# Performance work log

Measured on AMD Instinct MI355X. Metric: run time of the kernel, lower is better.

The kernel has to match this reference:

```python
import jax, jax.numpy as jnp
import numpy as np
from jax import lax

B, T, I, H = 64, 2048, 64, 256


def setup_inputs() -> dict:
    key = jax.random.key(0)
    ks = jax.random.split(key, 7)
    s = 1.0 / np.sqrt(H)  # PyTorch LSTM/Linear init scale
    x = jax.random.normal(ks[0], (B, T, I), dtype=jnp.float32)
    W_ih = jax.random.uniform(ks[1], (4 * H, I), minval=-s, maxval=s, dtype=jnp.float32)
    W_hh = jax.random.uniform(ks[2], (4 * H, H), minval=-s, maxval=s, dtype=jnp.float32)
    b_ih = jax.random.uniform(ks[3], (4 * H,), minval=-s, maxval=s, dtype=jnp.float32)
    b_hh = jax.random.uniform(ks[4], (4 * H,), minval=-s, maxval=s, dtype=jnp.float32)
    W_o = jax.random.uniform(ks[5], (1, H), minval=-s, maxval=s, dtype=jnp.float32)
    b_o = jax.random.uniform(ks[6], (1,), minval=-s, maxval=s, dtype=jnp.float32)
    return {"x": x, "W_ih": W_ih, "W_hh": W_hh, "b_ih": b_ih, "b_hh": b_hh, "W_o": W_o, "b_o": b_o}


def _lstm(x, W_ih, W_hh, b_ih, b_hh):
    # x: [B, T, I]. PyTorch gate order: i, f, g, o.
    Bn, Tn, _ = x.shape
    Hn = W_hh.shape[1]
    # Precompute input contribution for all timesteps (one big GEMM).
    gx = jnp.einsum('bti,gi->btg', x, W_ih) + b_ih + b_hh  # [B, T, 4H]

    def step(carry, gxt):
        h, c = carry
        gates = gxt + h @ W_hh.T  # [B, 4H]
        i, f, g, o = jnp.split(gates, 4, axis=-1)
        c = jax.nn.sigmoid(f) * c + jax.nn.sigmoid(i) * jnp.tanh(g)
        h = jax.nn.sigmoid(o) * jnp.tanh(c)
        return (h, c), h

    h0 = jnp.zeros((Bn, Hn), x.dtype)
    (_, _), hs = lax.scan(step, (h0, h0), jnp.swapaxes(gx, 0, 1))  # hs: [T, B, H]
    return jnp.swapaxes(hs, 0, 1)  # [B, T, H]


def reference(x, W_ih, W_hh, b_ih, b_hh, W_o, b_o):
    hs = _lstm(x, W_ih, W_hh, b_ih, b_hh)          # [B, T, H]
    return hs @ W_o.T + b_o                         # [B, T, 1]
```

## Files before the change

### kernel.cpp

```cpp
#include <hip/hip_runtime.h>
#include <hip/hip_fp16.h>

#define B_  64
#define T_  2048
#define I_  64
#define H_  256
#define G4_ 1024

typedef _Float16 h2v __attribute__((ext_vector_type(2)));

__device__ __forceinline__ float fdot2(uint32_t a, uint32_t b, float c) {
#if __has_builtin(__builtin_amdgcn_fdot2)
    return __builtin_amdgcn_fdot2(__builtin_bit_cast(h2v, a), __builtin_bit_cast(h2v, b), c, false);
#else
    h2v ha = __builtin_bit_cast(h2v, a), hb = __builtin_bit_cast(h2v, b);
    return c + (float)ha.x * (float)hb.x + (float)ha.y * (float)hb.y;
#endif
}

__device__ __forceinline__ ushort f2h(float v) {
    return __builtin_bit_cast(ushort, (_Float16)v);
}
__device__ __forceinline__ float h2f(ushort v) {
    return (float)__builtin_bit_cast(_Float16, v);
}

__global__ void repack_kernel(const float* __restrict__ Whh, ushort* __restrict__ wpk) {
    int o  = blockIdx.x * 256 + threadIdx.x;
    int j  = o & 7;
    int h  = (o >> 3) & 255;
    int kc = (o >> 11) & 31;
    int g  = o >> 16;
    float v = Whh[(g * 256 + h) * 256 + kc * 8 + j];
    wpk[o] = f2h(v);
}

__global__ __launch_bounds__(256) void gx_kernel(
    const float* __restrict__ x, const float* __restrict__ Wih,
    const float* __restrict__ bih, const float* __restrict__ bhh,
    ushort* __restrict__ gx, int t0, int TCc) {

    __shared__ float xs[32][64];
    const int bt0 = blockIdx.x * 32;
    const int row = blockIdx.y * 256 + threadIdx.x;

    for (int i = threadIdx.x; i < 512; i += 256) {
        int r  = i >> 4, c4 = i & 15;
        int bt = bt0 + r;
        int b  = bt / TCc;
        int tl = bt - b * TCc;
        *(float4*)(&xs[r][c4 * 4]) =
            *(const float4*)(&x[(((size_t)b * T_) + t0 + tl) * I_ + c4 * 4]);
    }
    __syncthreads();

    float w[64];
#pragma unroll
    for (int k = 0; k < 64; ++k) w[k] = Wih[row * I_ + k];
    const float bias = bih[row] + bhh[row];

    for (int i = 0; i < 32; ++i) {
        float acc = bias;
#pragma unroll
        for (int k4 = 0; k4 < 16; ++k4) {
            float4 xq = *(const float4*)(&xs[i][k4 * 4]);
            acc = fmaf(w[k4 * 4 + 0], xq.x, acc);
            acc = fmaf(w[k4 * 4 + 1], xq.y, acc);
            acc = fmaf(w[k4 * 4 + 2], xq.z, acc);
            acc = fmaf(w[k4 * 4 + 3], xq.w, acc);
        }
        gx[(size_t)(bt0 + i) * G4_ + row] = f2h(acc);
    }
}

__global__ __attribute__((amdgpu_flat_work_group_size(512, 512), amdgpu_waves_per_eu(2, 2)))
void lstm_kernel(
    const ushort* __restrict__ wpk, const ushort* __restrict__ gx,
    ushort* __restrict__ hbuf,
    float* __restrict__ state,
    int TCc, int first) {

    __shared__ __align__(16) ushort wg4[256 * 256];
    __shared__ __align__(16) ushort hs[256];
    __shared__ __align__(16) float pex[256][4];

    const int tid   = threadIdx.x;
    const int hd    = tid & 255;
    const int q     = tid >> 8;
    const int kbase = q << 4;
    const int tmask = hd & 31;
    const int b     = blockIdx.x;
    const bool q0   = (q == 0);

    uint32_t wi[64], wf[64], wg[64];
#pragma unroll
    for (int k = 0; k < 16; ++k) {
        uint4 v = *(const uint4*)(wpk + (size_t)(0 * 32 + kbase + k) * 2048 + hd * 8);
        wi[k * 4 + 0] = v.x; wi[k * 4 + 1] = v.y; wi[k * 4 + 2] = v.z; wi[k * 4 + 3] = v.w;
    }
#pragma unroll
    for (int k = 0; k < 16; ++k) {
        uint4 v = *(const uint4*)(wpk + (size_t)(1 * 32 + kbase + k) * 2048 + hd * 8);
        wf[k * 4 + 0] = v.x; wf[k * 4 + 1] = v.y; wf[k * 4 + 2] = v.z; wf[k * 4 + 3] = v.w;
    }
#pragma unroll
    for (int k = 0; k < 16; ++k) {
        uint4 v = *(const uint4*)(wpk + (size_t)(2 * 32 + kbase + k) * 2048 + hd * 8);
        wg[k * 4 + 0] = v.x; wg[k * 4 + 1] = v.y; wg[k * 4 + 2] = v.z; wg[k * 4 + 3] = v.w;
    }
#pragma unroll
    for (int k = 0; k < 16; ++k) {
        uint4 v = *(const uint4*)(wpk + (size_t)(3 * 32 + kbase + k) * 2048 + hd * 8);
        int u = (kbase + k) ^ tmask;
        *(uint4*)(wg4 + hd * 256 + u * 8) = v;
    }

    float c = 0.f, h = 0.f;
    if (q0) {
        if (!first) {
            c = state[b * H_ + hd];
            h = state[B_ * H_ + b * H_ + hd];
        }
        hs[hd] = f2h(h);
    }
    __syncthreads();

    const ushort* gxb = gx + (size_t)b * TCc * G4_;
    ushort* hb = hbuf + (size_t)b * TCc * H_;

    ushort c_i = 0, c_f = 0, c_g = 0, c_o = 0;
    if (q0) {
        c_i = gxb[hd]; c_f = gxb[256 + hd]; c_g = gxb[512 + hd]; c_o = gxb[768 + hd];
    }

    for (int tl = 0; tl < TCc; ++tl) {
        ushort n_i = 0, n_f = 0, n_g = 0, n_o = 0;
        if (q0) {
            const int tn = (tl + 1 < TCc) ? tl + 1 : tl;
            const size_t nb = (size_t)tn * G4_;
            n_i = gxb[nb + hd];       n_f = gxb[nb + 256 + hd];
            n_g = gxb[nb + 512 + hd]; n_o = gxb[nb + 768 + hd];
        }

        float ai, af, ag, ao;
        if (q0) { ai = h2f(c_i); af = h2f(c_f); ag = h2f(c_g); ao = h2f(c_o); }
        else    { ai = 0.f; af = 0.f; ag = 0.f; ao = 0.f; }

#pragma unroll
        for (int k = 0; k < 16; ++k) {
            const int kc = kbase + k;
            uint4 hq = *(const uint4*)(hs + kc * 8);
            int u = kc ^ tmask;
            uint4 wo = *(const uint4*)(wg4 + hd * 256 + u * 8);
            ai = fdot2(wi[k * 4 + 0], hq.x, ai);
            ai = fdot2(wi[k * 4 + 1], hq.y, ai);
            ai = fdot2(wi[k * 4 + 2], hq.z, ai);
            ai = fdot2(wi[k * 4 + 3], hq.w, ai);
            af = fdot2(wf[k * 4 + 0], hq.x, af);
            af = fdot2(wf[k * 4 + 1], hq.y, af);
            af = fdot2(wf[k * 4 + 2], hq.z, af);
            af = fdot2(wf[k * 4 + 3], hq.w, af);
            ag = fdot2(wg[k * 4 + 0], hq.x, ag);
            ag = fdot2(wg[k * 4 + 1], hq.y, ag);
            ag = fdot2(wg[k * 4 + 2], hq.z, ag);
            ag = fdot2(wg[k * 4 + 3], hq.w, ag);
            ao = fdot2(wo.x, hq.x, ao);
            ao = fdot2(wo.y, hq.y, ao);
            ao = fdot2(wo.z, hq.z, ao);
            ao = fdot2(wo.w, hq.w, ao);
        }

        if (!q0) {
            pex[hd][0] = ai; pex[hd][1] = af; pex[hd][2] = ag; pex[hd][3] = ao;
        }
        __syncthreads();

        if (q0) {
            float4 px = *(const float4*)(&pex[hd][0]);
            ai += px.x; af += px.y; ag += px.z; ao += px.w;

            float si = __builtin_amdgcn_rcpf(1.f + __expf(-ai));
            float sf = __builtin_amdgcn_rcpf(1.f + __expf(-af));
            float so = __builtin_amdgcn_rcpf(1.f + __expf(-ao));
            float eg = __expf(2.f * ag);
            float tg = (eg - 1.f) * __builtin_amdgcn_rcpf(eg + 1.f);
            c = sf * c + si * tg;
            float ec = __expf(2.f * c);
            float tc = (ec - 1.f) * __builtin_amdgcn_rcpf(ec + 1.f);
            h = so * tc;

            ushort hh = f2h(h);
            hs[hd] = hh;
            hb[(size_t)tl * H_ + hd] = hh;
        }
        __syncthreads();

        c_i = n_i; c_f = n_f; c_g = n_g; c_o = n_o;
    }

    if (q0) {
        state[b * H_ + hd]            = c;
        state[B_ * H_ + b * H_ + hd]  = h;
    }
}

__global__ __launch_bounds__(256) void proj_kernel(
    const ushort* __restrict__ hbuf, const float* __restrict__ Wo,
    const float* __restrict__ bo, float* __restrict__ out, int t0, int TCc) {

    const int lane = threadIdx.x & 63;
    const int wid  = blockIdx.x * 4 + (threadIdx.x >> 6);
    const int nw   = gridDim.x * 4;
    const int rows = B_ * TCc;

    float4 w = *(const float4*)(Wo + lane * 4);
    const float bov = bo[0];

    for (int r = wid; r < rows; r += nw) {
        const ushort* hp = hbuf + (size_t)r * H_ + lane * 4;
        ushort4 u = *(const ushort4*)hp;
        float p = h2f(u.x) * w.x + h2f(u.y) * w.y + h2f(u.z) * w.z + h2f(u.w) * w.w;
#pragma unroll
        for (int m = 1; m < 64; m <<= 1) p += __shfl_xor(p, m, 64);
        if (lane == 0) {
            int b  = r / TCc;
            int tl = r - b * TCc;
            out[(size_t)b * T_ + t0 + tl] = p + bov;
        }
    }
}

extern "C" void kernel_launch(void* const* d_in, const int* in_sizes, int n_in,
                              void* d_out, int out_size, void* d_ws, size_t ws_size,
                              hipStream_t stream) {
    const float* x   = (const float*)d_in[0];
    const float* Wih = (const float*)d_in[1];
    const float* Whh = (const float*)d_in[2];
    const float* bih = (const float*)d_in[3];
    const float* bhh = (const float*)d_in[4];
    const float* Wo  = (const float*)d_in[5];
    const float* bo  = (const float*)d_in[6];
    float* out = (float*)d_out;

    char* ws = (char*)d_ws;
    ushort* wpk   = (ushort*)ws;
    float*  state = (float*)(ws + 512 * 1024);
    char*   dyn   = ws + 640 * 1024;

    size_t avail = (ws_size > 640 * 1024) ? ws_size - 640 * 1024 : 0;
    long long tcmax = (long long)(avail / ((size_t)B_ * (G4_ + H_) * 2));
    int TC = (tcmax > T_) ? T_ : (int)tcmax;
    TC &= ~63;
    if (TC < 64) TC = 64;

    repack_kernel<<<1024, 256, 0, stream>>>(Whh, wpk);

    for (int t0 = 0; t0 < T_; t0 += TC) {
        int TCc = (T_ - t0 < TC) ? (T_ - t0) : TC;
        ushort* gxb  = (ushort*)dyn;
        ushort* hbuf = (ushort*)(dyn + (size_t)B_ * TCc * G4_ * 2);
        dim3 g1((B_ * TCc) / 32, 4);
        gx_kernel<<<g1, 256, 0, stream>>>(x, Wih, bih, bhh, gxb, t0, TCc);
        lstm_kernel<<<B_, 512, 0, stream>>>(wpk, gxb, hbuf, state, TCc, t0 == 0 ? 1 : 0);
        proj_kernel<<<256, 256, 0, stream>>>(hbuf, Wo, bo, out, t0, TCc);
    }
    (void)in_sizes; (void)n_in; (void)out_size;
}
```

Before: 3.448 ms.

## Move part of o-gate weights to registers and cap time chunk size

The o-gate weights are split so that 4 of each thread's 16 k-chunks sit in registers and the other 12 sit in LDS. The LDS layout changes from an XOR-swizzled per-row layout to a [k][q][hd] layout. This cuts per-step LDS reads for the o-gate and shrinks shared memory, at the cost of 16 more VGPRs per thread. The time chunk is also capped at 512 steps, so the gx/lstm/proj kernels run over several chunks instead of one, which may keep the gx buffer in cache but adds launches.

```diff
diff --git a/kernel.cpp b/kernel.cpp
--- a/kernel.cpp
+++ b/kernel.cpp
@@ -80,7 +80,7 @@
     float* __restrict__ state,
     int TCc, int first) {
 
-    __shared__ __align__(16) ushort wg4[256 * 256];
+    __shared__ __align__(16) ushort wg4[12 * 2 * 256 * 8];
     __shared__ __align__(16) ushort hs[256];
     __shared__ __align__(16) float pex[256][4];
 
@@ -88,7 +88,6 @@
     const int hd    = tid & 255;
     const int q     = tid >> 8;
     const int kbase = q << 4;
-    const int tmask = hd & 31;
     const int b     = blockIdx.x;
     const bool q0   = (q == 0);
 
@@ -109,10 +108,15 @@
         wg[k * 4 + 0] = v.x; wg[k * 4 + 1] = v.y; wg[k * 4 + 2] = v.z; wg[k * 4 + 3] = v.w;
     }
 #pragma unroll
-    for (int k = 0; k < 16; ++k) {
+    for (int k = 0; k < 12; ++k) {
         uint4 v = *(const uint4*)(wpk + (size_t)(3 * 32 + kbase + k) * 2048 + hd * 8);
-        int u = (kbase + k) ^ tmask;
-        *(uint4*)(wg4 + hd * 256 + u * 8) = v;
+        *(uint4*)(wg4 + ((k * 2 + q) * 256 + hd) * 8) = v;
+    }
+    uint32_t wo_r[16];
+#pragma unroll
+    for (int k = 0; k < 4; ++k) {
+        uint4 v = *(const uint4*)(wpk + (size_t)(3 * 32 + kbase + 12 + k) * 2048 + hd * 8);
+        wo_r[k * 4 + 0] = v.x; wo_r[k * 4 + 1] = v.y; wo_r[k * 4 + 2] = v.z; wo_r[k * 4 + 3] = v.w;
     }
 
     float c = 0.f, h = 0.f;
@@ -147,11 +151,10 @@
         else    { ai = 0.f; af = 0.f; ag = 0.f; ao = 0.f; }
 
 #pragma unroll
-        for (int k = 0; k < 16; ++k) {
+        for (int k = 0; k < 12; ++k) {
             const int kc = kbase + k;
             uint4 hq = *(const uint4*)(hs + kc * 8);
-            int u = kc ^ tmask;
-            uint4 wo = *(const uint4*)(wg4 + hd * 256 + u * 8);
+            uint4 wo = *(const uint4*)(wg4 + ((k * 2 + q) * 256 + hd) * 8);
             ai = fdot2(wi[k * 4 + 0], hq.x, ai);
             ai = fdot2(wi[k * 4 + 1], hq.y, ai);
             ai = fdot2(wi[k * 4 + 2], hq.z, ai);
@@ -169,6 +172,28 @@
             ao = fdot2(wo.z, hq.z, ao);
             ao = fdot2(wo.w, hq.w, ao);
         }
+#pragma unroll
+        for (int k = 12; k < 16; ++k) {
+            const int kc = kbase + k;
+            const int r  = (k - 12) * 4;
+            uint4 hq = *(const uint4*)(hs + kc * 8);
+            ai = fdot2(wi[k * 4 + 0], hq.x, ai);
+            ai = fdot2(wi[k * 4 + 1], hq.y, ai);
+            ai = fdot2(wi[k * 4 + 2], hq.z, ai);
+            ai = fdot2(wi[k * 4 + 3], hq.w, ai);
+            af = fdot2(wf[k * 4 + 0], hq.x, af);
+            af = fdot2(wf[k * 4 + 1], hq.y, af);
+            af = fdot2(wf[k * 4 + 2], hq.z, af);
+            af = fdot2(wf[k * 4 + 3], hq.w, af);
+            ag = fdot2(wg[k * 4 + 0], hq.x, ag);
+            ag = fdot2(wg[k * 4 + 1], hq.y, ag);
+            ag = fdot2(wg[k * 4 + 2], hq.z, ag);
+            ag = fdot2(wg[k * 4 + 3], hq.w, ag);
+            ao = fdot2(wo_r[r + 0], hq.x, ao);
+            ao = fdot2(wo_r[r + 1], hq.y, ao);
+            ao = fdot2(wo_r[r + 2], hq.z, ao);
+            ao = fdot2(wo_r[r + 3], hq.w, ao);
+        }
 
         if (!q0) {
             pex[hd][0] = ai; pex[hd][1] = af; pex[hd][2] = ag; pex[hd][3] = ao;
@@ -249,7 +274,7 @@
 
     size_t avail = (ws_size > 640 * 1024) ? ws_size - 640 * 1024 : 0;
     long long tcmax = (long long)(avail / ((size_t)B_ * (G4_ + H_) * 2));
-    int TC = (tcmax > T_) ? T_ : (int)tcmax;
+    int TC = (tcmax > 512) ? 512 : (int)tcmax;
     TC &= ~63;
     if (TC < 64) TC = 64;
 
```

Result: slower. 3.878 ms (+12.5%).

## Split LSTM K-reduction across 4 lanes with shuffles and double-buffered hidden state

Applied to the files above, without the earlier changes.

Each recurrent block now uses 1024 threads: four adjacent lanes share one hidden unit and each covers a quarter of K. Their partial dot products are combined with wave shuffles instead of a shared-memory exchange, which removes one barrier per timestep. The hidden state is double-buffered in padded shared memory, and the gate preactivations are stored interleaved so each thread reads all four with one 8-byte load. The time chunk is capped at 512, giving more kernel launches, and every lane now computes the redundant activation math.

```diff
diff --git a/kernel.cpp b/kernel.cpp
--- a/kernel.cpp
+++ b/kernel.cpp
@@ -38,11 +38,12 @@
 __global__ __launch_bounds__(256) void gx_kernel(
     const float* __restrict__ x, const float* __restrict__ Wih,
     const float* __restrict__ bih, const float* __restrict__ bhh,
-    ushort* __restrict__ gx, int t0, int TCc) {
+    ushort* __restrict__ gx2, int t0, int TCc) {
 
     __shared__ float xs[32][64];
     const int bt0 = blockIdx.x * 32;
-    const int row = blockIdx.y * 256 + threadIdx.x;
+    const int gq  = blockIdx.y;
+    const int row = gq * 256 + threadIdx.x;
 
     for (int i = threadIdx.x; i < 512; i += 256) {
         int r  = i >> 4, c4 = i & 15;
@@ -69,138 +70,126 @@
             acc = fmaf(w[k4 * 4 + 2], xq.z, acc);
             acc = fmaf(w[k4 * 4 + 3], xq.w, acc);
         }
-        gx[(size_t)(bt0 + i) * G4_ + row] = f2h(acc);
-    }
-}
-
-__global__ __attribute__((amdgpu_flat_work_group_size(512, 512), amdgpu_waves_per_eu(2, 2)))
+        gx2[((size_t)(bt0 + i) * 256 + threadIdx.x) * 4 + gq] = f2h(acc);
+    }
+}
+
+__global__ __attribute__((amdgpu_flat_work_group_size(1024, 1024)))
 void lstm_kernel(
-    const ushort* __restrict__ wpk, const ushort* __restrict__ gx,
+    const ushort* __restrict__ wpk, const ushort* __restrict__ gx2,
     ushort* __restrict__ hbuf,
     float* __restrict__ state,
     int TCc, int first) {
 
     __shared__ __align__(16) ushort wg4[256 * 256];
-    __shared__ __align__(16) ushort hs[256];
-    __shared__ __align__(16) float pex[256][4];
-
-    const int tid   = threadIdx.x;
-    const int hd    = tid & 255;
-    const int q     = tid >> 8;
-    const int kbase = q << 4;
-    const int tmask = hd & 31;
-    const int b     = blockIdx.x;
-    const bool q0   = (q == 0);
-
-    uint32_t wi[64], wf[64], wg[64];
-#pragma unroll
-    for (int k = 0; k < 16; ++k) {
-        uint4 v = *(const uint4*)(wpk + (size_t)(0 * 32 + kbase + k) * 2048 + hd * 8);
+    __shared__ __align__(16) ushort hs[2][288];
+
+    const int tid = threadIdx.x;
+    const int q   = tid & 3;
+    const int hd  = tid >> 2;
+    const int hm  = hd & 31;
+    const int b   = blockIdx.x;
+
+    uint32_t wi[32], wf[32], wg[32];
+#pragma unroll
+    for (int k = 0; k < 8; ++k) {
+        uint4 v = *(const uint4*)(wpk + (size_t)(0 * 32 + q * 8 + k) * 2048 + hd * 8);
         wi[k * 4 + 0] = v.x; wi[k * 4 + 1] = v.y; wi[k * 4 + 2] = v.z; wi[k * 4 + 3] = v.w;
     }
 #pragma unroll
-    for (int k = 0; k < 16; ++k) {
-        uint4 v = *(const uint4*)(wpk + (size_t)(1 * 32 + kbase + k) * 2048 + hd * 8);
+    for (int k = 0; k < 8; ++k) {
+        uint4 v = *(const uint4*)(wpk + (size_t)(1 * 32 + q * 8 + k) * 2048 + hd * 8);
         wf[k * 4 + 0] = v.x; wf[k * 4 + 1] = v.y; wf[k * 4 + 2] = v.z; wf[k * 4 + 3] = v.w;
     }
 #pragma unroll
-    for (int k = 0; k < 16; ++k) {
-        uint4 v = *(const uint4*)(wpk + (size_t)(2 * 32 + kbase + k) * 2048 + hd * 8);
+    for (int k = 0; k < 8; ++k) {
+        uint4 v = *(const uint4*)(wpk + (size_t)(2 * 32 + q * 8 + k) * 2048 + hd * 8);
         wg[k * 4 + 0] = v.x; wg[k * 4 + 1] = v.y; wg[k * 4 + 2] = v.z; wg[k * 4 + 3] = v.w;
     }
 #pragma unroll
-    for (int k = 0; k < 16; ++k) {
-        uint4 v = *(const uint4*)(wpk + (size_t)(3 * 32 + kbase + k) * 2048 + hd * 8);
-        int u = (kbase + k) ^ tmask;
+    for (int k = 0; k < 8; ++k) {
+        uint4 v = *(const uint4*)(wpk + (size_t)(3 * 32 + q * 8 + k) * 2048 + hd * 8);
+        int u = (q * 8 + k) ^ hm;
         *(uint4*)(wg4 + hd * 256 + u * 8) = v;
     }
 
     float c = 0.f, h = 0.f;
-    if (q0) {
-        if (!first) {
-            c = state[b * H_ + hd];
-            h = state[B_ * H_ + b * H_ + hd];
-        }
-        hs[hd] = f2h(h);
+    if (!first) {
+        c = state[b * H_ + hd];
+        h = state[B_ * H_ + b * H_ + hd];
+    }
+    if (q == 0) {
+        int sw = ((hd >> 3) + (hd >> 6)) * 8 + (hd & 7);
+        hs[0][sw] = f2h(h);
     }
     __syncthreads();
 
-    const ushort* gxb = gx + (size_t)b * TCc * G4_;
+    const ushort* gxb = gx2 + (size_t)b * TCc * G4_;
     ushort* hb = hbuf + (size_t)b * TCc * H_;
 
-    ushort c_i = 0, c_f = 0, c_g = 0, c_o = 0;
-    if (q0) {
-        c_i = gxb[hd]; c_f = gxb[256 + hd]; c_g = gxb[512 + hd]; c_o = gxb[768 + hd];
-    }
+    ushort4 cg = *(const ushort4*)(gxb + (size_t)0 * G4_ + hd * 4);
 
     for (int tl = 0; tl < TCc; ++tl) {
-        ushort n_i = 0, n_f = 0, n_g = 0, n_o = 0;
-        if (q0) {
-            const int tn = (tl + 1 < TCc) ? tl + 1 : tl;
-            const size_t nb = (size_t)tn * G4_;
-            n_i = gxb[nb + hd];       n_f = gxb[nb + 256 + hd];
-            n_g = gxb[nb + 512 + hd]; n_o = gxb[nb + 768 + hd];
-        }
-
-        float ai, af, ag, ao;
-        if (q0) { ai = h2f(c_i); af = h2f(c_f); ag = h2f(c_g); ao = h2f(c_o); }
-        else    { ai = 0.f; af = 0.f; ag = 0.f; ao = 0.f; }
-
-#pragma unroll
-        for (int k = 0; k < 16; ++k) {
-            const int kc = kbase + k;
-            uint4 hq = *(const uint4*)(hs + kc * 8);
-            int u = kc ^ tmask;
+        const int tn = (tl + 1 < TCc) ? tl + 1 : tl;
+        ushort4 ng = *(const ushort4*)(gxb + (size_t)tn * G4_ + hd * 4);
+
+        const ushort* hsr = hs[tl & 1];
+        float ai = 0.f, af = 0.f, agv = 0.f, ao = 0.f;
+
+#pragma unroll
+        for (int k = 0; k < 8; ++k) {
+            uint4 hq = *(const uint4*)(hsr + (q * 9 + k) * 8);
+            int u = (q * 8 + k) ^ hm;
             uint4 wo = *(const uint4*)(wg4 + hd * 256 + u * 8);
-            ai = fdot2(wi[k * 4 + 0], hq.x, ai);
-            ai = fdot2(wi[k * 4 + 1], hq.y, ai);
-            ai = fdot2(wi[k * 4 + 2], hq.z, ai);
-            ai = fdot2(wi[k * 4 + 3], hq.w, ai);
-            af = fdot2(wf[k * 4 + 0], hq.x, af);
-            af = fdot2(wf[k * 4 + 1], hq.y, af);
-            af = fdot2(wf[k * 4 + 2], hq.z, af);
-            af = fdot2(wf[k * 4 + 3], hq.w, af);
-            ag = fdot2(wg[k * 4 + 0], hq.x, ag);
-            ag = fdot2(wg[k * 4 + 1], hq.y, ag);
-            ag = fdot2(wg[k * 4 + 2], hq.z, ag);
-            ag = fdot2(wg[k * 4 + 3], hq.w, ag);
-            ao = fdot2(wo.x, hq.x, ao);
-            ao = fdot2(wo.y, hq.y, ao);
-            ao = fdot2(wo.z, hq.z, ao);
-            ao = fdot2(wo.w, hq.w, ao);
-        }
-
-        if (!q0) {
-            pex[hd][0] = ai; pex[hd][1] = af; pex[hd][2] = ag; pex[hd][3] = ao;
+            ai  = fdot2(wi[k * 4 + 0], hq.x, ai);
+            ai  = fdot2(wi[k * 4 + 1], hq.y, ai);
+            ai  = fdot2(wi[k * 4 + 2], hq.z, ai);
+            ai  = fdot2(wi[k * 4 + 3], hq.w, ai);
+            af  = fdot2(wf[k * 4 + 0], hq.x, af);
+            af  = fdot2(wf[k * 4 + 1], hq.y, af);
+            af  = fdot2(wf[k * 4 + 2], hq.z, af);
+            af  = fdot2(wf[k * 4 + 3], hq.w, af);
+            agv = fdot2(wg[k * 4 + 0], hq.x, agv);
+            agv = fdot2(wg[k * 4 + 1], hq.y, agv);
+            agv = fdot2(wg[k * 4 + 2], hq.z, agv);
+            agv = fdot2(wg[k * 4 + 3], hq.w, agv);
+            ao  = fdot2(wo.x, hq.x, ao);
+            ao  = fdot2(wo.y, hq.y, ao);
+            ao  = fdot2(wo.z, hq.z, ao);
+            ao  = fdot2(wo.w, hq.w, ao);
+        }
+
+        ai  += __shfl_xor(ai, 1);  ai  += __shfl_xor(ai, 2);
+        af  += __shfl_xor(af, 1);  af  += __shfl_xor(af, 2);
+        agv += __shfl_xor(agv, 1); agv += __shfl_xor(agv, 2);
+        ao  += __shfl_xor(ao, 1);  ao  += __shfl_xor(ao, 2);
+
+        ai += h2f(cg.x); af += h2f(cg.y); agv += h2f(cg.z); ao += h2f(cg.w);
+
+        float si = __builtin_amdgcn_rcpf(1.f + __expf(-ai));
+        float sf = __builtin_amdgcn_rcpf(1.f + __expf(-af));
+        float so = __builtin_amdgcn_rcpf(1.f + __expf(-ao));
+        float eg = __expf(2.f * agv);
+        float tg = (eg - 1.f) * __builtin_amdgcn_rcpf(eg + 1.f);
+        c = sf * c + si * tg;
+        float ec = __expf(2.f * c);
+        float tc = (ec - 1.f) * __builtin_amdgcn_rcpf(ec + 1.f);
+        h = so * tc;
+
+        if (q == 0) {
+            ushort hh = f2h(h);
+            int sw = ((hd >> 3) + (hd >> 6)) * 8 + (hd & 7);
+            hs[(tl + 1) & 1][sw] = hh;
+            hb[(size_t)tl * H_ + hd] = hh;
         }
         __syncthreads();
 
-        if (q0) {
-            float4 px = *(const float4*)(&pex[hd][0]);
-            ai += px.x; af += px.y; ag += px.z; ao += px.w;
-
-            float si = __builtin_amdgcn_rcpf(1.f + __expf(-ai));
-            float sf = __builtin_amdgcn_rcpf(1.f + __expf(-af));
-            float so = __builtin_amdgcn_rcpf(1.f + __expf(-ao));
-            float eg = __expf(2.f * ag);
-            float tg = (eg - 1.f) * __builtin_amdgcn_rcpf(eg + 1.f);
-            c = sf * c + si * tg;
-            float ec = __expf(2.f * c);
-            float tc = (ec - 1.f) * __builtin_amdgcn_rcpf(ec + 1.f);
-            h = so * tc;
-
-            ushort hh = f2h(h);
-            hs[hd] = hh;
-            hb[(size_t)tl * H_ + hd] = hh;
-        }
-        __syncthreads();
-
-        c_i = n_i; c_f = n_f; c_g = n_g; c_o = n_o;
-    }
-
-    if (q0) {
-        state[b * H_ + hd]            = c;
-        state[B_ * H_ + b * H_ + hd]  = h;
+        cg = ng;
+    }
+
+    if (q == 0) {
+        state[b * H_ + hd]           = c;
+        state[B_ * H_ + b * H_ + hd] = h;
     }
 }
 
@@ -249,7 +238,7 @@
 
     size_t avail = (ws_size > 640 * 1024) ? ws_size - 640 * 1024 : 0;
     long long tcmax = (long long)(avail / ((size_t)B_ * (G4_ + H_) * 2));
-    int TC = (tcmax > T_) ? T_ : (int)tcmax;
+    int TC = (tcmax > 512) ? 512 : (int)tcmax;
     TC &= ~63;
     if (TC < 64) TC = 64;
 
@@ -261,7 +250,7 @@
         ushort* hbuf = (ushort*)(dyn + (size_t)B_ * TCc * G4_ * 2);
         dim3 g1((B_ * TCc) / 32, 4);
         gx_kernel<<<g1, 256, 0, stream>>>(x, Wih, bih, bhh, gxb, t0, TCc);
-        lstm_kernel<<<B_, 512, 0, stream>>>(wpk, gxb, hbuf, state, TCc, t0 == 0 ? 1 : 0);
+        lstm_kernel<<<B_, 1024, 0, stream>>>(wpk, gxb, hbuf, state, TCc, t0 == 0 ? 1 : 0);
         proj_kernel<<<256, 256, 0, stream>>>(hbuf, Wo, bo, out, t0, TCc);
     }
     (void)in_sizes; (void)n_in; (void)out_size;
```

Result: slower. 4.086 ms (+18.5%).
